# Kernel tuning notes

Hardware: AMD Instinct MI355X
Metric: run time of the kernel (lower is better)

The kernel has to match this reference:

```python
import jax, jax.numpy as jnp
import numpy as np

LN_EPS = 1e-5

def setup_inputs() -> dict:
    key = jax.random.key(0)
    ks = jax.random.split(key, 5)
    B, S, Dv, Dl, V = 4, 576, 1024, 4096, 32000
    return {
        "vision_feats": jax.random.normal(ks[0], (B, S, Dv), dtype=jnp.float32),
        "W1_w": jax.random.normal(ks[1], (Dl, Dv), dtype=jnp.float32) * (Dv ** -0.5),
        "W1_b": jax.random.normal(ks[2], (Dl,), dtype=jnp.float32) * 0.02,
        "W2_w": jax.random.normal(ks[3], (V, Dl), dtype=jnp.float32) * (Dl ** -0.5),
        "llm_token_embed": jax.random.normal(ks[4], (V, Dl), dtype=jnp.float32) * 0.02,
    }

def reference(vision_feats, W1_w, W1_b, W2_w, llm_token_embed):
    # W1: (B,S,Dv) @ (Dv,Dl) + b -> (B,S,Dl)
    x = jnp.einsum('bsd,ed->bse', vision_feats, W1_w) + W1_b
    # layer_norm over last dim, no affine params
    mu = jnp.mean(x, axis=-1, keepdims=True)
    var = jnp.mean(jnp.square(x - mu), axis=-1, keepdims=True)
    xn = (x - mu) * jax.lax.rsqrt(var + LN_EPS)
    # W2 (no bias): (B,S,Dl) -> (B,S,V) vocab logits
    logits = jnp.einsum('bse,ve->bsv', xn, W2_w)
    P = jax.nn.softmax(logits, axis=-1)
    # softmax-weighted mixture of LLM token embeddings: (B,S,V) @ (V,Dl)
    F_align = jnp.einsum('bsv,ve->bse', P, llm_token_embed)
    return F_align
```

## Files before the change

kernel.cpp:

```cpp
#include <hip/hip_runtime.h>
#include <hip/hip_bf16.h>
#include <stdint.h>

typedef __bf16 bf16_t;
typedef __attribute__((ext_vector_type(8))) __bf16 bf16x8;
typedef __attribute__((ext_vector_type(4))) __bf16 bf16x4;
typedef __attribute__((ext_vector_type(4))) float f32x4;
typedef __attribute__((ext_vector_type(8))) unsigned short u16x8;

#define M_TOK 2304
#define DV    1024
#define DLAT  4096
#define VOCAB 32000

__device__ __forceinline__ float bf2f(unsigned short u) {
  union { unsigned int i; float f; } v; v.i = ((unsigned int)u) << 16; return v.f;
}
__device__ __forceinline__ bf16_t f2bf(float f) { return (bf16_t)f; }

#define GLOAD16(gp, lp) \
  __builtin_amdgcn_global_load_lds( \
      (const __attribute__((address_space(1))) unsigned int*)(const void*)(gp), \
      (__attribute__((address_space(3))) unsigned int*)(void*)(lp), 16, 0, 0)

constexpr int GBM = 128, GBN = 128, GBK = 32;

template<int EPI>
__global__ void __launch_bounds__(256, 3)
gemm_bb(const bf16_t* __restrict__ Ap, const bf16_t* __restrict__ Bp,
        void* __restrict__ Cp, void* __restrict__ Cp2,
        const float* __restrict__ bias,
        int Ksplit, int ld, int ldc, int Mt, int Nt)
{
  __shared__ __align__(16) bf16_t Al[3][GBM * GBK];
  __shared__ __align__(16) bf16_t Bl[3][GBN * GBK];

  const int nwg = gridDim.x;
  const int orig = blockIdx.x;
  const int q = nwg >> 3, r = nwg & 7;
  const int xcd = orig & 7, idx = orig >> 3;
  const int wg = (xcd < r ? xcd * (q + 1) : r * (q + 1) + (xcd - r) * q) + idx;
  const int mt = wg % Mt;
  const int nt = (wg / Mt) % Nt;
  const int sp = wg / (Mt * Nt);
  const int m0 = mt * GBM, n0 = nt * GBN;
  const int kbase = sp * Ksplit;

  const int t    = threadIdx.x;
  const int lane = t & 63, wv = t >> 6;
  const int wm = wv >> 1, wn = wv & 1;
  const int lr = lane & 15, kc = lane >> 4;

  f32x4 acc[4][4];
#pragma unroll
  for (int i = 0; i < 4; ++i)
#pragma unroll
    for (int j = 0; j < 4; ++j)
#pragma unroll
      for (int x = 0; x < 4; ++x) acc[i][j][x] = 0.0f;

  const int rql = lane >> 2;
  const int cbs = (((lane & 3) ^ ((lane >> 3) & 3)) * 16);
  const int sw8 = (kc ^ ((lr >> 1) & 3)) * 8;
  const size_t rstride = (size_t)ld * 2;

  const int NT = Ksplit / GBK;

  auto STAGE = [&](int kt, int nb) {
    const size_t kb = (size_t)(kbase + kt * GBK) * 2;
    const char* ga = (const char*)Ap + (size_t)(m0 + wv * 32 + rql) * rstride + kb + cbs;
    char* la = (char*)&Al[nb][0] + wv * 2048;
    GLOAD16(ga, la);
    GLOAD16(ga + 16 * rstride, la + 1024);
    const char* gb = (const char*)Bp + (size_t)(n0 + wv * 32 + rql) * rstride + kb + cbs;
    char* lb = (char*)&Bl[nb][0] + wv * 2048;
    GLOAD16(gb, lb);
    GLOAD16(gb + 16 * rstride, lb + 1024);
  };

  auto COMPUTE = [&](int nb) {
    bf16x8 af[4], bfv[4];
#pragma unroll
    for (int f = 0; f < 4; ++f)
      af[f] = *(const bf16x8*)(&Al[nb][(wm * 64 + f * 16 + lr) * GBK + sw8]);
#pragma unroll
    for (int f = 0; f < 4; ++f)
      bfv[f] = *(const bf16x8*)(&Bl[nb][(wn * 64 + f * 16 + lr) * GBK + sw8]);
    __builtin_amdgcn_s_setprio(1);
#pragma unroll
    for (int i = 0; i < 4; ++i)
#pragma unroll
      for (int j = 0; j < 4; ++j)
        acc[i][j] = __builtin_amdgcn_mfma_f32_16x16x32_bf16(af[i], bfv[j], acc[i][j], 0, 0, 0);
    __builtin_amdgcn_s_setprio(0);
  };

  auto BARX = [&]() {
    asm volatile("s_waitcnt lgkmcnt(0)" ::: "memory");
    __builtin_amdgcn_s_barrier();
  };

  STAGE(0, 0);
  STAGE(1, 1);
  asm volatile("s_waitcnt vmcnt(4)" ::: "memory");
  __builtin_amdgcn_s_barrier();

  int bc = 0, bn = 1, bs = 2;
  for (int kt = 0; kt < NT - 2; ++kt) {
    STAGE(kt + 2, bs);
    COMPUTE(bc);
    asm volatile("s_waitcnt vmcnt(4)" ::: "memory");
    BARX();
    const int tmp = bc; bc = bn; bn = bs; bs = tmp;
  }
  COMPUTE(bc);
  asm volatile("s_waitcnt vmcnt(0)" ::: "memory");
  BARX();
  COMPUTE(bn);

  float* Cf = (EPI == 2) ? (sp == 0 ? (float*)Cp : (float*)Cp2) : (float*)Cp;
#pragma unroll
  for (int j = 0; j < 4; ++j) {
    const int col = n0 + wn * 64 + j * 16 + lr;
    float bv = 0.0f;
    if (EPI == 0) bv = bias[col];
#pragma unroll
    for (int i = 0; i < 4; ++i) {
      const int row = m0 + wm * 64 + i * 16 + kc * 4;
      f32x4 a4 = acc[i][j];
      if (EPI == 1) {
        bf16_t* C = (bf16_t*)Cp;
#pragma unroll
        for (int x = 0; x < 4; ++x) C[(size_t)(row + x) * ldc + col] = f2bf(a4[x]);
      } else if (EPI == 0) {
#pragma unroll
        for (int x = 0; x < 4; ++x) Cf[(size_t)(row + x) * ldc + col] = a4[x] + bv;
      } else {
#pragma unroll
        for (int x = 0; x < 4; ++x) Cf[(size_t)(row + x) * ldc + col] = a4[x];
      }
    }
  }
}

__global__ void __launch_bounds__(256)
addk(float* __restrict__ out, const float* __restrict__ part, int n4)
{
  const int stride = gridDim.x * 256;
  for (int i = blockIdx.x * 256 + threadIdx.x; i < n4; i += stride) {
    f32x4 a = *(const f32x4*)(out + i * 4);
    f32x4 b = *(const f32x4*)(part + i * 4);
#pragma unroll
    for (int x = 0; x < 4; ++x) a[x] += b[x];
    *(f32x4*)(out + i * 4) = a;
  }
}

__global__ void __launch_bounds__(256)
cvt_bf16_k(const float* __restrict__ in, bf16_t* __restrict__ out, long n8)
{
  const long stride = (long)gridDim.x * 256;
  for (long i = (long)blockIdx.x * 256 + threadIdx.x; i < n8; i += stride) {
    f32x4 a = *(const f32x4*)(in + i * 8);
    f32x4 b = *(const f32x4*)(in + i * 8 + 4);
    bf16x8 o;
#pragma unroll
    for (int j = 0; j < 4; ++j) { o[j] = f2bf(a[j]); o[j + 4] = f2bf(b[j]); }
    *(bf16x8*)(out + i * 8) = o;
  }
}

__global__ void __launch_bounds__(256)
embT_k(const float* __restrict__ E, bf16_t* __restrict__ ET)
{
  __shared__ bf16_t tl[64][72];
  const int vb = blockIdx.x % (VOCAB / 64);
  const int eb = blockIdx.x / (VOCAB / 64);
  const int v0 = vb * 64, e0 = eb * 64;
  const int t = threadIdx.x;

  const int rr = t >> 4, c4 = (t & 15) * 4;
#pragma unroll
  for (int p = 0; p < 4; ++p) {
    const float* src = E + (size_t)(v0 + rr + p * 16) * DLAT + e0 + c4;
    f32x4 a = *(const f32x4*)src;
#pragma unroll
    for (int j = 0; j < 4; ++j) tl[c4 + j][rr + p * 16] = f2bf(a[j]);
  }
  __syncthreads();

  const int el = t >> 3, v8 = (t & 7) * 8;
#pragma unroll
  for (int p = 0; p < 2; ++p) {
    bf16x8 o = *(const bf16x8*)(&tl[el + p * 32][v8]);
    *(bf16x8*)(ET + (size_t)(e0 + el + p * 32) * VOCAB + v0 + v8) = o;
  }
}

__global__ void __launch_bounds__(256)
ln_k(const float* __restrict__ x, bf16_t* __restrict__ xn)
{
  __shared__ float sm[4];
  const int row = blockIdx.x, t = threadIdx.x;
  const float* xr = x + (size_t)row * DLAT;
  f32x4 v[4];
#pragma unroll
  for (int i = 0; i < 4; ++i) v[i] = *(const f32x4*)(xr + (t + i * 256) * 4);

  float s = 0.0f;
#pragma unroll
  for (int i = 0; i < 4; ++i)
#pragma unroll
    for (int j = 0; j < 4; ++j) s += v[i][j];
#pragma unroll
  for (int o = 32; o > 0; o >>= 1) s += __shfl_xor(s, o, 64);
  if ((t & 63) == 0) sm[t >> 6] = s;
  __syncthreads();
  const float mean = (sm[0] + sm[1] + sm[2] + sm[3]) * (1.0f / DLAT);
  __syncthreads();

  float qv = 0.0f;
#pragma unroll
  for (int i = 0; i < 4; ++i)
#pragma unroll
    for (int j = 0; j < 4; ++j) { float d = v[i][j] - mean; qv += d * d; }
#pragma unroll
  for (int o = 32; o > 0; o >>= 1) qv += __shfl_xor(qv, o, 64);
  if ((t & 63) == 0) sm[t >> 6] = qv;
  __syncthreads();
  const float varr = (sm[0] + sm[1] + sm[2] + sm[3]) * (1.0f / DLAT);
  const float rs = rsqrtf(varr + 1e-5f);

  bf16_t* outr = xn + (size_t)row * DLAT;
#pragma unroll
  for (int i = 0; i < 4; ++i) {
    bf16x4 o;
#pragma unroll
    for (int j = 0; j < 4; ++j) o[j] = f2bf((v[i][j] - mean) * rs);
    *(bf16x4*)(outr + (t + i * 256) * 4) = o;
  }
}

__global__ void __launch_bounds__(256)
softmax_k(bf16_t* __restrict__ L)
{
  __shared__ __align__(16) bf16_t rs_[VOCAB];
  __shared__ float sm[4];
  const int row = blockIdx.x, t = threadIdx.x;
  bf16_t* lrow = L + (size_t)row * VOCAB;
  const int NF = VOCAB / 8;

  float m = -3.0e38f;
  for (int f = t; f < NF; f += 256) {
    u16x8 u = *(const u16x8*)(&lrow[f * 8]);
    *(u16x8*)(&rs_[f * 8]) = u;
#pragma unroll
    for (int j = 0; j < 8; ++j) m = fmaxf(m, bf2f(u[j]));
  }
#pragma unroll
  for (int o = 32; o > 0; o >>= 1) m = fmaxf(m, __shfl_xor(m, o, 64));
  if ((t & 63) == 0) sm[t >> 6] = m;
  __syncthreads();
  m = fmaxf(fmaxf(sm[0], sm[1]), fmaxf(sm[2], sm[3]));
  __syncthreads();

  float s = 0.0f;
  for (int f = t; f < NF; f += 256) {
    u16x8 u = *(const u16x8*)(&rs_[f * 8]);
#pragma unroll
    for (int j = 0; j < 8; ++j) s += __expf(bf2f(u[j]) - m);
  }
#pragma unroll
  for (int o = 32; o > 0; o >>= 1) s += __shfl_xor(s, o, 64);
  if ((t & 63) == 0) sm[t >> 6] = s;
  __syncthreads();
  const float inv = 1.0f / (sm[0] + sm[1] + sm[2] + sm[3]);

  for (int f = t; f < NF; f += 256) {
    u16x8 u = *(const u16x8*)(&rs_[f * 8]);
    bf16x8 o;
#pragma unroll
    for (int j = 0; j < 8; ++j) o[j] = f2bf(__expf(bf2f(u[j]) - m) * inv);
    *(bf16x8*)(&lrow[f * 8]) = o;
  }
}

extern "C" void kernel_launch(void* const* d_in, const int* in_sizes, int n_in,
                              void* d_out, int out_size, void* d_ws, size_t ws_size,
                              hipStream_t stream)
{
  (void)in_sizes; (void)n_in; (void)out_size; (void)ws_size;
  const float* vision = (const float*)d_in[0];
  const float* W1w    = (const float*)d_in[1];
  const float* W1b    = (const float*)d_in[2];
  const float* W2w    = (const float*)d_in[3];
  const float* Emb    = (const float*)d_in[4];
  float* out = (float*)d_out;

  char* ws = (char*)d_ws;
  bf16_t* xn     = (bf16_t*)ws;
  bf16_t* logits = (bf16_t*)(ws + 18874368);
  float*  xbuf   = (float*)(ws + 166330368);
  bf16_t* wslot  = (bf16_t*)(ws + 204079104);
  bf16_t* xnv    = (bf16_t*)(ws + 466223104);
  bf16_t* w1b    = (bf16_t*)(ws + 470941696);

  cvt_bf16_k<<<dim3(512), dim3(256), 0, stream>>>(vision, xnv, (long)M_TOK * DV / 8);
  cvt_bf16_k<<<dim3(512), dim3(256), 0, stream>>>(W1w, w1b, (long)DLAT * DV / 8);

  gemm_bb<0><<<dim3(18 * 32), dim3(256), 0, stream>>>(
      xnv, w1b, xbuf, nullptr, W1b, DV, DV, DLAT, 18, 32);

  ln_k<<<dim3(M_TOK), dim3(256), 0, stream>>>(xbuf, xn);

  cvt_bf16_k<<<dim3(2048), dim3(256), 0, stream>>>(W2w, wslot, (long)VOCAB * DLAT / 8);

  gemm_bb<1><<<dim3(18 * 250), dim3(256), 0, stream>>>(
      xn, wslot, logits, nullptr, nullptr, DLAT, DLAT, VOCAB, 18, 250);

  embT_k<<<dim3((VOCAB / 64) * (DLAT / 64)), dim3(256), 0, stream>>>(Emb, wslot);

  softmax_k<<<dim3(M_TOK), dim3(256), 0, stream>>>(logits);

  gemm_bb<2><<<dim3(18 * 32 * 2), dim3(256), 0, stream>>>(
      logits, wslot, out, xbuf, nullptr, VOCAB / 2, VOCAB, DLAT, 18, 32);

  addk<<<dim3(1024), dim3(256), 0, stream>>>(out, xbuf, (M_TOK * DLAT) / 4);
}
```

Before: 1.956 ms.

## Store logits and transposed embeddings in pre-swizzled tile-packed layout for final GEMM

The logits GEMM epilogue and the embedding transpose kernel now write their outputs directly in a tile-packed layout of 128x32 bf16 tiles with the LDS XOR swizzle already applied. The softmax kernel reads and writes through that same layout. The final GEMM then stages each tile with contiguous 16-byte loads instead of strided row loads, improving coalescing and TLB behaviour on the largest GEMM. In exchange, the epilogue writes scattered 2-byte stores and softmax row accesses become strided across tiles.

Result: slower. 2.028 ms (+3.7%).

```diff
diff --git a/kernel.cpp b/kernel.cpp
--- a/kernel.cpp
+++ b/kernel.cpp
@@ -12,6 +12,7 @@
 #define DV    1024
 #define DLAT  4096
 #define VOCAB 32000
+#define NTKV  1000
 
 __device__ __forceinline__ float bf2f(unsigned short u) {
   union { unsigned int i; float f; } v; v.i = ((unsigned int)u) << 16; return v.f;
@@ -23,14 +24,15 @@
       (const __attribute__((address_space(1))) unsigned int*)(const void*)(gp), \
       (__attribute__((address_space(3))) unsigned int*)(void*)(lp), 16, 0, 0)
 
+
 constexpr int GBM = 128, GBN = 128, GBK = 32;
 
-template<int EPI>
+template<int EPI, bool PACKED>
 __global__ void __launch_bounds__(256, 3)
 gemm_bb(const bf16_t* __restrict__ Ap, const bf16_t* __restrict__ Bp,
         void* __restrict__ Cp, void* __restrict__ Cp2,
         const float* __restrict__ bias,
-        int Ksplit, int ld, int ldc, int Mt, int Nt)
+        int Ksplit, int ld, int ldc, int Mt, int Nt, int ntk)
 {
   __shared__ __align__(16) bf16_t Al[3][GBM * GBK];
   __shared__ __align__(16) bf16_t Bl[3][GBN * GBK];
@@ -45,6 +47,7 @@
   const int sp = wg / (Mt * Nt);
   const int m0 = mt * GBM, n0 = nt * GBN;
   const int kbase = sp * Ksplit;
+  const int ktile0 = kbase >> 5;
 
   const int t    = threadIdx.x;
   const int lane = t & 63, wv = t >> 6;
@@ -67,15 +70,29 @@
   const int NT = Ksplit / GBK;
 
   auto STAGE = [&](int kt, int nb) {
-    const size_t kb = (size_t)(kbase + kt * GBK) * 2;
-    const char* ga = (const char*)Ap + (size_t)(m0 + wv * 32 + rql) * rstride + kb + cbs;
-    char* la = (char*)&Al[nb][0] + wv * 2048;
-    GLOAD16(ga, la);
-    GLOAD16(ga + 16 * rstride, la + 1024);
-    const char* gb = (const char*)Bp + (size_t)(n0 + wv * 32 + rql) * rstride + kb + cbs;
-    char* lb = (char*)&Bl[nb][0] + wv * 2048;
-    GLOAD16(gb, lb);
-    GLOAD16(gb + 16 * rstride, lb + 1024);
+    if constexpr (PACKED) {
+      const size_t tk = (size_t)(ktile0 + kt);
+      const char* ga = (const char*)Ap + ((size_t)mt * ntk + tk) * 8192
+                       + wv * 2048 + lane * 16;
+      char* la = (char*)&Al[nb][0] + wv * 2048;
+      GLOAD16(ga, la);
+      GLOAD16(ga + 1024, la + 1024);
+      const char* gb = (const char*)Bp + ((size_t)nt * ntk + tk) * 8192
+                       + wv * 2048 + lane * 16;
+      char* lb = (char*)&Bl[nb][0] + wv * 2048;
+      GLOAD16(gb, lb);
+      GLOAD16(gb + 1024, lb + 1024);
+    } else {
+      const size_t kb = (size_t)(kbase + kt * GBK) * 2;
+      const char* ga = (const char*)Ap + (size_t)(m0 + wv * 32 + rql) * rstride + kb + cbs;
+      char* la = (char*)&Al[nb][0] + wv * 2048;
+      GLOAD16(ga, la);
+      GLOAD16(ga + 16 * rstride, la + 1024);
+      const char* gb = (const char*)Bp + (size_t)(n0 + wv * 32 + rql) * rstride + kb + cbs;
+      char* lb = (char*)&Bl[nb][0] + wv * 2048;
+      GLOAD16(gb, lb);
+      GLOAD16(gb + 16 * rstride, lb + 1024);
+    }
   };
 
   auto COMPUTE = [&](int nb) {
@@ -135,9 +152,21 @@
       } else if (EPI == 0) {
 #pragma unroll
         for (int x = 0; x < 4; ++x) Cf[(size_t)(row + x) * ldc + col] = a4[x] + bv;
+      } else if (EPI == 2) {
+#pragma unroll
+        for (int x = 0; x < 4; ++x) Cf[(size_t)(row + x) * ldc + col] = a4[x];
       } else {
-#pragma unroll
-        for (int x = 0; x < 4; ++x) Cf[(size_t)(row + x) * ldc + col] = a4[x];
+        bf16_t* C = (bf16_t*)Cp;
+        const int vt = col >> 5;
+        const int sg = (col & 31) >> 3;
+        const int klo = col & 7;
+        const size_t mtb = ((size_t)(row >> 7) * ldc + vt) * 4096;
+#pragma unroll
+        for (int x = 0; x < 4; ++x) {
+          const int rr_ = (row + x) & 127;
+          const int sp_ = sg ^ ((rr_ >> 1) & 3);
+          C[mtb + rr_ * 32 + sp_ * 8 + klo] = f2bf(a4[x]);
+        }
       }
     }
   }
@@ -171,7 +200,7 @@
 }
 
 __global__ void __launch_bounds__(256)
-embT_k(const float* __restrict__ E, bf16_t* __restrict__ ET)
+embP_k(const float* __restrict__ E, bf16_t* __restrict__ ET)
 {
   __shared__ bf16_t tl[64][72];
   const int vb = blockIdx.x % (VOCAB / 64);
@@ -190,10 +219,15 @@
   __syncthreads();
 
   const int el = t >> 3, v8 = (t & 7) * 8;
+  const int vt = vb * 2 + ((t & 7) >> 2);
+  const int sg = t & 3;
 #pragma unroll
   for (int p = 0; p < 2; ++p) {
+    const int e = e0 + el + p * 32;
+    const int nt_ = e >> 7, r_ = e & 127;
+    const int sp_ = sg ^ ((r_ >> 1) & 3);
     bf16x8 o = *(const bf16x8*)(&tl[el + p * 32][v8]);
-    *(bf16x8*)(ET + (size_t)(e0 + el + p * 32) * VOCAB + v0 + v8) = o;
+    *(bf16x8*)(&ET[((size_t)nt_ * NTKV + vt) * 4096 + r_ * 32 + sp_ * 8]) = o;
   }
 }
 
@@ -247,12 +281,13 @@
   __shared__ __align__(16) bf16_t rs_[VOCAB];
   __shared__ float sm[4];
   const int row = blockIdx.x, t = threadIdx.x;
-  bf16_t* lrow = L + (size_t)row * VOCAB;
+  const int mt_ = row >> 7, r_ = row & 127, rx = (r_ >> 1) & 3;
+  bf16_t* base = L + ((size_t)mt_ * NTKV) * 4096 + r_ * 32;
   const int NF = VOCAB / 8;
 
   float m = -3.0e38f;
   for (int f = t; f < NF; f += 256) {
-    u16x8 u = *(const u16x8*)(&lrow[f * 8]);
+    u16x8 u = *(const u16x8*)(base + (size_t)(f >> 2) * 4096 + ((f & 3) ^ rx) * 8);
     *(u16x8*)(&rs_[f * 8]) = u;
 #pragma unroll
     for (int j = 0; j < 8; ++j) m = fmaxf(m, bf2f(u[j]));
@@ -281,7 +316,7 @@
     bf16x8 o;
 #pragma unroll
     for (int j = 0; j < 8; ++j) o[j] = f2bf(__expf(bf2f(u[j]) - m) * inv);
-    *(bf16x8*)(&lrow[f * 8]) = o;
+    *(bf16x8*)(base + (size_t)(f >> 2) * 4096 + ((f & 3) ^ rx) * 8) = o;
   }
 }
 
@@ -308,22 +343,22 @@
   cvt_bf16_k<<<dim3(512), dim3(256), 0, stream>>>(vision, xnv, (long)M_TOK * DV / 8);
   cvt_bf16_k<<<dim3(512), dim3(256), 0, stream>>>(W1w, w1b, (long)DLAT * DV / 8);
 
-  gemm_bb<0><<<dim3(18 * 32), dim3(256), 0, stream>>>(
-      xnv, w1b, xbuf, nullptr, W1b, DV, DV, DLAT, 18, 32);
+  gemm_bb<0, false><<<dim3(18 * 32), dim3(256), 0, stream>>>(
+      xnv, w1b, xbuf, nullptr, W1b, DV, DV, DLAT, 18, 32, 0);
 
   ln_k<<<dim3(M_TOK), dim3(256), 0, stream>>>(xbuf, xn);
 
   cvt_bf16_k<<<dim3(2048), dim3(256), 0, stream>>>(W2w, wslot, (long)VOCAB * DLAT / 8);
 
-  gemm_bb<1><<<dim3(18 * 250), dim3(256), 0, stream>>>(
-      xn, wslot, logits, nullptr, nullptr, DLAT, DLAT, VOCAB, 18, 250);
-
-  embT_k<<<dim3((VOCAB / 64) * (DLAT / 64)), dim3(256), 0, stream>>>(Emb, wslot);
+  gemm_bb<3, false><<<dim3(18 * 250), dim3(256), 0, stream>>>(
+      xn, wslot, logits, nullptr, nullptr, DLAT, DLAT, NTKV, 18, 250, 0);
+
+  embP_k<<<dim3((VOCAB / 64) * (DLAT / 64)), dim3(256), 0, stream>>>(Emb, wslot);
 
   softmax_k<<<dim3(M_TOK), dim3(256), 0, stream>>>(logits);
 
-  gemm_bb<2><<<dim3(18 * 32 * 2), dim3(256), 0, stream>>>(
-      logits, wslot, out, xbuf, nullptr, VOCAB / 2, VOCAB, DLAT, 18, 32);
+  gemm_bb<2, true><<<dim3(18 * 32 * 2), dim3(256), 0, stream>>>(
+      logits, wslot, out, xbuf, nullptr, VOCAB / 2, 0, DLAT, 18, 32, NTKV);
 
   addk<<<dim3(1024), dim3(256), 0, stream>>>(out, xbuf, (M_TOK * DLAT) / 4);
 }
```

## Use 512-thread 256-row GEMM tiles for logits and embedding mix with split-K 4

Applied to the files above, without the earlier changes.

Adds a 512-thread GEMM kernel with 256xBN output tiles (BN 256 or 128), so each block reuses A and B tiles across more output and needs fewer global loads per FLOP. The logits GEMM and the final P@Emb GEMM now use it, the final one with a 4-way split-K into extra workspace buffers followed by a 3-way reduction kernel. A 2-way split-K fallback is kept for when the workspace is too small. The larger tiles raise register use and cut block count, which may hurt occupancy or tail balance. The added partial buffers also mean more reduction traffic.

Result: slower. 2.301 ms (+17.6%).

```diff
diff --git a/kernel.cpp b/kernel.cpp
--- a/kernel.cpp
+++ b/kernel.cpp
@@ -23,17 +23,19 @@
       (const __attribute__((address_space(1))) unsigned int*)(const void*)(gp), \
       (__attribute__((address_space(3))) unsigned int*)(void*)(lp), 16, 0, 0)
 
-constexpr int GBM = 128, GBN = 128, GBK = 32;
-
-template<int EPI>
-__global__ void __launch_bounds__(256, 3)
-gemm_bb(const bf16_t* __restrict__ Ap, const bf16_t* __restrict__ Bp,
+template<int BN_, int EPI>
+__global__ void __launch_bounds__(512, (BN_ == 128 ? 4 : 2))
+gemm512(const bf16_t* __restrict__ Ap, const bf16_t* __restrict__ Bp,
         void* __restrict__ Cp, void* __restrict__ Cp2,
-        const float* __restrict__ bias,
+        void* __restrict__ Cp3, void* __restrict__ Cp4,
         int Ksplit, int ld, int ldc, int Mt, int Nt)
 {
-  __shared__ __align__(16) bf16_t Al[3][GBM * GBK];
-  __shared__ __align__(16) bf16_t Bl[3][GBN * GBK];
+  constexpr int WMR = (BN_ == 128) ? 64 : 128;
+  constexpr int NFM = WMR / 16;
+  constexpr int LW  = (BN_ == 128) ? 3 : 4;
+
+  __shared__ __align__(16) bf16_t Al[3][256 * 32];
+  __shared__ __align__(16) bf16_t Bl[3][BN_ * 32];
 
   const int nwg = gridDim.x;
   const int orig = blockIdx.x;
@@ -43,8 +45,133 @@
   const int mt = wg % Mt;
   const int nt = (wg / Mt) % Nt;
   const int sp = wg / (Mt * Nt);
+  const int m0 = mt * 256, n0 = nt * BN_;
+  const int kbase = sp * Ksplit;
+
+  const int t    = threadIdx.x;
+  const int lane = t & 63, wv = t >> 6;
+  const int wm = (BN_ == 128) ? (wv >> 1) : (wv >> 2);
+  const int wn = (BN_ == 128) ? (wv & 1)  : (wv & 3);
+  const int lr = lane & 15, kc = lane >> 4;
+
+  f32x4 acc[NFM][4];
+#pragma unroll
+  for (int i = 0; i < NFM; ++i)
+#pragma unroll
+    for (int j = 0; j < 4; ++j)
+#pragma unroll
+      for (int x = 0; x < 4; ++x) acc[i][j][x] = 0.0f;
+
+  const int rql = lane >> 2;
+  const int cbs = (((lane & 3) ^ ((lane >> 3) & 3)) * 16);
+  const int sw8 = (kc ^ ((lr >> 1) & 3)) * 8;
+  const size_t rstride = (size_t)ld * 2;
+
+  const int NT = Ksplit / 32;
+
+  auto STAGE = [&](int kt, int nb) {
+    const size_t kb = (size_t)(kbase + kt * 32) * 2;
+    const char* ga = (const char*)Ap + (size_t)(m0 + wv * 32 + rql) * rstride + kb + cbs;
+    char* la = (char*)&Al[nb][0] + wv * 2048;
+    GLOAD16(ga, la);
+    GLOAD16(ga + 16 * rstride, la + 1024);
+    if constexpr (BN_ == 256) {
+      const char* gb = (const char*)Bp + (size_t)(n0 + wv * 32 + rql) * rstride + kb + cbs;
+      char* lb = (char*)&Bl[nb][0] + wv * 2048;
+      GLOAD16(gb, lb);
+      GLOAD16(gb + 16 * rstride, lb + 1024);
+    } else {
+      const char* gb = (const char*)Bp + (size_t)(n0 + wv * 16 + rql) * rstride + kb + cbs;
+      char* lb = (char*)&Bl[nb][0] + wv * 1024;
+      GLOAD16(gb, lb);
+    }
+  };
+
+  auto COMPUTE = [&](int nb) {
+    bf16x8 af[NFM], bfv[4];
+#pragma unroll
+    for (int f = 0; f < NFM; ++f)
+      af[f] = *(const bf16x8*)(&Al[nb][(wm * WMR + f * 16 + lr) * 32 + sw8]);
+#pragma unroll
+    for (int f = 0; f < 4; ++f)
+      bfv[f] = *(const bf16x8*)(&Bl[nb][(wn * 64 + f * 16 + lr) * 32 + sw8]);
+    __builtin_amdgcn_s_setprio(1);
+#pragma unroll
+    for (int i = 0; i < NFM; ++i)
+#pragma unroll
+      for (int j = 0; j < 4; ++j)
+        acc[i][j] = __builtin_amdgcn_mfma_f32_16x16x32_bf16(af[i], bfv[j], acc[i][j], 0, 0, 0);
+    __builtin_amdgcn_s_setprio(0);
+  };
+
+  auto WAITL = [&]() {
+    if constexpr (LW == 3) asm volatile("s_waitcnt vmcnt(3)" ::: "memory");
+    else                   asm volatile("s_waitcnt vmcnt(4)" ::: "memory");
+  };
+  auto BARX = [&]() {
+    asm volatile("s_waitcnt lgkmcnt(0)" ::: "memory");
+    __builtin_amdgcn_s_barrier();
+  };
+
+  STAGE(0, 0);
+  STAGE(1, 1);
+  WAITL();
+  __builtin_amdgcn_s_barrier();
+
+  int bc = 0, bn = 1, bs = 2;
+  for (int kt = 0; kt < NT - 2; ++kt) {
+    STAGE(kt + 2, bs);
+    COMPUTE(bc);
+    WAITL();
+    BARX();
+    const int tmp = bc; bc = bn; bn = bs; bs = tmp;
+  }
+  COMPUTE(bc);
+  asm volatile("s_waitcnt vmcnt(0)" ::: "memory");
+  BARX();
+  COMPUTE(bn);
+
+  float* Cf = nullptr;
+  if (EPI == 2)
+    Cf = (sp == 0) ? (float*)Cp : (sp == 1) ? (float*)Cp2
+       : (sp == 2) ? (float*)Cp3 : (float*)Cp4;
+#pragma unroll
+  for (int j = 0; j < 4; ++j) {
+    const int col = n0 + wn * 64 + j * 16 + lr;
+#pragma unroll
+    for (int i = 0; i < NFM; ++i) {
+      const int row = m0 + wm * WMR + i * 16 + kc * 4;
+      f32x4 a4 = acc[i][j];
+      if (EPI == 1) {
+        bf16_t* C = (bf16_t*)Cp;
+#pragma unroll
+        for (int x = 0; x < 4; ++x) C[(size_t)(row + x) * ldc + col] = f2bf(a4[x]);
+      } else {
+#pragma unroll
+        for (int x = 0; x < 4; ++x) Cf[(size_t)(row + x) * ldc + col] = a4[x];
+      }
+    }
+  }
+}
+
+constexpr int GBM = 128, GBN = 128, GBK = 32;
+
+template<int EPI>
+__global__ void __launch_bounds__(256, 3)
+gemm_bb(const bf16_t* __restrict__ Ap, const bf16_t* __restrict__ Bp,
+        void* __restrict__ Cp, const float* __restrict__ bias,
+        int K, int ld, int ldc, int Mt)
+{
+  __shared__ __align__(16) bf16_t Al[3][GBM * GBK];
+  __shared__ __align__(16) bf16_t Bl[3][GBN * GBK];
+
+  const int nwg = gridDim.x;
+  const int orig = blockIdx.x;
+  const int q = nwg >> 3, r = nwg & 7;
+  const int xcd = orig & 7, idx = orig >> 3;
+  const int wg = (xcd < r ? xcd * (q + 1) : r * (q + 1) + (xcd - r) * q) + idx;
+  const int mt = wg % Mt, nt = wg / Mt;
   const int m0 = mt * GBM, n0 = nt * GBN;
-  const int kbase = sp * Ksplit;
 
   const int t    = threadIdx.x;
   const int lane = t & 63, wv = t >> 6;
@@ -64,10 +191,10 @@
   const int sw8 = (kc ^ ((lr >> 1) & 3)) * 8;
   const size_t rstride = (size_t)ld * 2;
 
-  const int NT = Ksplit / GBK;
+  const int NT = K / GBK;
 
   auto STAGE = [&](int kt, int nb) {
-    const size_t kb = (size_t)(kbase + kt * GBK) * 2;
+    const size_t kb = (size_t)kt * GBK * 2;
     const char* ga = (const char*)Ap + (size_t)(m0 + wv * 32 + rql) * rstride + kb + cbs;
     char* la = (char*)&Al[nb][0] + wv * 2048;
     GLOAD16(ga, la);
@@ -118,27 +245,17 @@
   BARX();
   COMPUTE(bn);
 
-  float* Cf = (EPI == 2) ? (sp == 0 ? (float*)Cp : (float*)Cp2) : (float*)Cp;
 #pragma unroll
   for (int j = 0; j < 4; ++j) {
     const int col = n0 + wn * 64 + j * 16 + lr;
-    float bv = 0.0f;
-    if (EPI == 0) bv = bias[col];
+    const float bv = (EPI == 0) ? bias[col] : 0.0f;
 #pragma unroll
     for (int i = 0; i < 4; ++i) {
       const int row = m0 + wm * 64 + i * 16 + kc * 4;
       f32x4 a4 = acc[i][j];
-      if (EPI == 1) {
-        bf16_t* C = (bf16_t*)Cp;
-#pragma unroll
-        for (int x = 0; x < 4; ++x) C[(size_t)(row + x) * ldc + col] = f2bf(a4[x]);
-      } else if (EPI == 0) {
-#pragma unroll
-        for (int x = 0; x < 4; ++x) Cf[(size_t)(row + x) * ldc + col] = a4[x] + bv;
-      } else {
-#pragma unroll
-        for (int x = 0; x < 4; ++x) Cf[(size_t)(row + x) * ldc + col] = a4[x];
-      }
+      float* C = (float*)Cp;
+#pragma unroll
+      for (int x = 0; x < 4; ++x) C[(size_t)(row + x) * ldc + col] = a4[x] + bv;
     }
   }
 }
@@ -152,6 +269,22 @@
     f32x4 b = *(const f32x4*)(part + i * 4);
 #pragma unroll
     for (int x = 0; x < 4; ++x) a[x] += b[x];
+    *(f32x4*)(out + i * 4) = a;
+  }
+}
+
+__global__ void __launch_bounds__(256)
+addk3(float* __restrict__ out, const float* __restrict__ pa,
+      const float* __restrict__ pb, const float* __restrict__ pc, int n4)
+{
+  const int stride = gridDim.x * 256;
+  for (int i = blockIdx.x * 256 + threadIdx.x; i < n4; i += stride) {
+    f32x4 a = *(const f32x4*)(out + i * 4);
+    f32x4 b = *(const f32x4*)(pa + i * 4);
+    f32x4 c = *(const f32x4*)(pb + i * 4);
+    f32x4 d = *(const f32x4*)(pc + i * 4);
+#pragma unroll
+    for (int x = 0; x < 4; ++x) a[x] += b[x] + c[x] + d[x];
     *(f32x4*)(out + i * 4) = a;
   }
 }
@@ -289,7 +422,7 @@
                               void* d_out, int out_size, void* d_ws, size_t ws_size,
                               hipStream_t stream)
 {
-  (void)in_sizes; (void)n_in; (void)out_size; (void)ws_size;
+  (void)in_sizes; (void)n_in; (void)out_size;
   const float* vision = (const float*)d_in[0];
   const float* W1w    = (const float*)d_in[1];
   const float* W1b    = (const float*)d_in[2];
@@ -302,28 +435,36 @@
   bf16_t* logits = (bf16_t*)(ws + 18874368);
   float*  xbuf   = (float*)(ws + 166330368);
   bf16_t* wslot  = (bf16_t*)(ws + 204079104);
-  bf16_t* xnv    = (bf16_t*)(ws + 466223104);
-  bf16_t* w1b    = (bf16_t*)(ws + 470941696);
+  bf16_t* xnv    = (bf16_t*)(ws + 204079104);
+  bf16_t* w1b    = (bf16_t*)(ws + 208797696);
+  float*  p2     = (float*)(ws + 466223104);
+  float*  p3     = (float*)(ws + 503971840);
+  const size_t NEED_BIG = 541720576ull;
 
   cvt_bf16_k<<<dim3(512), dim3(256), 0, stream>>>(vision, xnv, (long)M_TOK * DV / 8);
   cvt_bf16_k<<<dim3(512), dim3(256), 0, stream>>>(W1w, w1b, (long)DLAT * DV / 8);
 
   gemm_bb<0><<<dim3(18 * 32), dim3(256), 0, stream>>>(
-      xnv, w1b, xbuf, nullptr, W1b, DV, DV, DLAT, 18, 32);
+      xnv, w1b, xbuf, W1b, DV, DV, DLAT, 18);
 
   ln_k<<<dim3(M_TOK), dim3(256), 0, stream>>>(xbuf, xn);
 
   cvt_bf16_k<<<dim3(2048), dim3(256), 0, stream>>>(W2w, wslot, (long)VOCAB * DLAT / 8);
 
-  gemm_bb<1><<<dim3(18 * 250), dim3(256), 0, stream>>>(
-      xn, wslot, logits, nullptr, nullptr, DLAT, DLAT, VOCAB, 18, 250);
+  gemm512<256, 1><<<dim3(9 * 125), dim3(512), 0, stream>>>(
+      xn, wslot, logits, nullptr, nullptr, nullptr, DLAT, DLAT, VOCAB, 9, 125);
 
   embT_k<<<dim3((VOCAB / 64) * (DLAT / 64)), dim3(256), 0, stream>>>(Emb, wslot);
 
   softmax_k<<<dim3(M_TOK), dim3(256), 0, stream>>>(logits);
 
-  gemm_bb<2><<<dim3(18 * 32 * 2), dim3(256), 0, stream>>>(
-      logits, wslot, out, xbuf, nullptr, VOCAB / 2, VOCAB, DLAT, 18, 32);
-
-  addk<<<dim3(1024), dim3(256), 0, stream>>>(out, xbuf, (M_TOK * DLAT) / 4);
-}
+  if (ws_size >= NEED_BIG) {
+    gemm512<256, 2><<<dim3(9 * 16 * 4), dim3(512), 0, stream>>>(
+        logits, wslot, out, xbuf, p2, p3, VOCAB / 4, VOCAB, DLAT, 9, 16);
+    addk3<<<dim3(1024), dim3(256), 0, stream>>>(out, xbuf, p2, p3, (M_TOK * DLAT) / 4);
+  } else {
+    gemm512<128, 2><<<dim3(9 * 32 * 2), dim3(512), 0, stream>>>(
+        logits, wslot, out, xbuf, nullptr, nullptr, VOCAB / 2, VOCAB, DLAT, 9, 32);
+    addk<<<dim3(1024), dim3(256), 0, stream>>>(out, xbuf, (M_TOK * DLAT) / 4);
+  }
+}
```
